# Kernel tuning notes

Hardware: AMD Instinct MI355X
Metric: run time of the kernel (lower is better)

The kernel has to match this reference:

```python
import jax, jax.numpy as jnp
import numpy as np

B, T, C, H = 4, 2048, 1024, 16
HD = C // H

def setup_inputs() -> dict:
    key = jax.random.key(0)
    ks = jax.random.split(key, 9)
    s = 1.0 / np.sqrt(C)
    return {
        'x':  jax.random.normal(ks[0], (B, T, C), jnp.float32),
        'Wq': jax.random.normal(ks[1], (C, C), jnp.float32) * s,
        'bq': jnp.zeros((C,), jnp.float32),
        'Wk': jax.random.normal(ks[2], (C, C), jnp.float32) * s,
        'bk': jnp.zeros((C,), jnp.float32),
        'Wv': jax.random.normal(ks[3], (C, C), jnp.float32) * s,
        'bv': jnp.zeros((C,), jnp.float32),
        'Wo': jax.random.normal(ks[4], (C, C), jnp.float32) * s,
        'bo': jnp.zeros((C,), jnp.float32),
    }

def reference(x, Wq, bq, Wk, bk, Wv, bv, Wo, bo):
    Bx, Tx, Cx = x.shape
    # projections (torch Linear: x @ W.T + b); split heads -> (B,H,T,HD)
    def heads(y):
        return y.reshape(Bx, Tx, H, HD).transpose(0, 2, 1, 3)
    q = heads(x @ Wq.T + bq)
    k = heads(x @ Wk.T + bk)
    v = heads(x @ Wv.T + bv)
    # NOTE: original scales by 1/sqrt(embedding_dim), not head_dim
    scale = 1.0 / jnp.sqrt(jnp.asarray(Cx, x.dtype))
    att = jnp.einsum('bhqd,bhkd->bhqk', q, k) * scale
    mask = jnp.tril(jnp.ones((Tx, Tx), dtype=bool))
    att = jnp.where(mask, att, jnp.asarray(-jnp.inf, att.dtype))
    att = jax.nn.softmax(att, axis=-1)
    y = jnp.einsum('bhqk,bhkd->bhqd', att, v)
    y = y.transpose(0, 2, 1, 3).reshape(Bx, Tx, Cx)
    return y @ Wo.T + bo
```

## Files before the change

### kernel.cpp

```cpp
#include <hip/hip_runtime.h>
#include <hip/hip_bf16.h>
#include <stdint.h>

#define NB 4
#define NT 2048
#define NC 1024
#define NH 16
#define NHD 64
#define NM (NB*NT)

typedef __attribute__((ext_vector_type(8))) __bf16 bf16x8;
typedef __attribute__((ext_vector_type(4))) float floatx4;
typedef __attribute__((ext_vector_type(8))) unsigned short ushortx8;

#define AS1(p) ((const __attribute__((address_space(1))) void*)(p))
#define AS3(p) ((__attribute__((address_space(3))) void*)(p))

__device__ __forceinline__ unsigned short f2bf(float f) {
    union { float f; unsigned int u; } v; v.f = f;
    unsigned int u = v.u;
    return (unsigned short)((u + 0x7FFFu + ((u >> 16) & 1u)) >> 16);
}
__device__ __forceinline__ unsigned int pk2(float lo, float hi) {
    union { float f; unsigned int u; } a, b; a.f = hi; b.f = lo;
    return __builtin_amdgcn_perm(a.u, b.u, 0x07060302u);
}


__global__ void cast_x_tiled(const float* __restrict__ in,
                             unsigned short* __restrict__ out, int ntiles) {
    const int wid  = (blockIdx.x * blockDim.x + threadIdx.x) >> 6;
    const int lane = threadIdx.x & 63;
    if (wid >= ntiles) return;
    const int R = wid >> 5, C = wid & 31;
    const float* src = in + ((size_t)(R*16 + (lane >> 2)))*1024 + C*32 + (lane & 3)*8;
    const floatx4 v0 = *(const floatx4*)src;
    const floatx4 v1 = *(const floatx4*)(src + 4);
    ushortx8 o;
    o[0] = f2bf(v0[0]); o[1] = f2bf(v0[1]); o[2] = f2bf(v0[2]); o[3] = f2bf(v0[3]);
    o[4] = f2bf(v1[0]); o[5] = f2bf(v1[1]); o[6] = f2bf(v1[2]); o[7] = f2bf(v1[3]);
    *(ushortx8*)&out[(size_t)wid*512 + (((lane & 3)*16 + (lane >> 2)))*8] = o;
}

__global__ void cast4_tiled(const float* __restrict__ w0, const float* __restrict__ w1,
                            const float* __restrict__ w2, const float* __restrict__ w3,
                            unsigned short* __restrict__ o0, unsigned short* __restrict__ o1,
                            unsigned short* __restrict__ o2, unsigned short* __restrict__ o3,
                            int ntiles) {
    const int wid  = (blockIdx.x * blockDim.x + threadIdx.x) >> 6;
    const int lane = threadIdx.x & 63;
    if (wid >= ntiles) return;
    const float* in; unsigned short* out;
    switch (blockIdx.y) {
        case 0: in = w0; out = o0; break;
        case 1: in = w1; out = o1; break;
        case 2: in = w2; out = o2; break;
        default: in = w3; out = o3; break;
    }
    const int R = wid >> 5, C = wid & 31;
    const float* src = in + ((size_t)(R*16 + (lane >> 2)))*1024 + C*32 + (lane & 3)*8;
    const floatx4 v0 = *(const floatx4*)src;
    const floatx4 v1 = *(const floatx4*)(src + 4);
    ushortx8 o;
    o[0] = f2bf(v0[0]); o[1] = f2bf(v0[1]); o[2] = f2bf(v0[2]); o[3] = f2bf(v0[3]);
    o[4] = f2bf(v1[0]); o[5] = f2bf(v1[1]); o[6] = f2bf(v1[2]); o[7] = f2bf(v1[3]);
    *(ushortx8*)&out[(size_t)wid*512 + (((lane & 3)*16 + (lane >> 2)))*8] = o;
}

#define TM 128
#define TN 128
#define BK 32

template<int MODE>
__device__ __forceinline__ void gemm_core(
    const unsigned short* __restrict__ A,
    const unsigned short* __restrict__ W,
    const float* __restrict__ bias,
    void* __restrict__ Out,
    unsigned short* As, unsigned short* Bs,
    int m_base, int n_base, float oscale)
{
    const int tid  = threadIdx.x;
    const int lane = tid & 63;
    const int wv   = tid >> 6;
    const int quad = lane >> 4;
    const int l16  = lane & 15;
    const int wm = (wv >> 1) * 64;
    const int wn = (wv & 1) * 64;

    floatx4 acc[4][4];
    #pragma unroll
    for (int i = 0; i < 4; ++i)
        #pragma unroll
        for (int j = 0; j < 4; ++j)
            acc[i][j] = (floatx4){0.f, 0.f, 0.f, 0.f};

    const int kTiles = NC / BK;
    const int kct = NC >> 5;

    const unsigned short* At = A + ((size_t)((m_base >> 4) + wv*2) * kct) * 512 + (size_t)lane*8;
    const unsigned short* Wt = W + ((size_t)((n_base >> 4) + wv*2) * kct) * 512 + (size_t)lane*8;
    const size_t rstride = (size_t)kct * 512;

    for (int kt = 0; kt < kTiles; ++kt) {
        __syncthreads();
        #pragma unroll
        for (int i = 0; i < 2; ++i) {
            __builtin_amdgcn_global_load_lds(
                AS1(At + (size_t)kt*512 + i*rstride),
                AS3(&As[(wv*2 + i)*512]), 16, 0, 0);
            __builtin_amdgcn_global_load_lds(
                AS1(Wt + (size_t)kt*512 + i*rstride),
                AS3(&Bs[(wv*2 + i)*512]), 16, 0, 0);
        }
        __syncthreads();

        bf16x8 af[4], bfr[4];
        #pragma unroll
        for (int mi = 0; mi < 4; ++mi)
            af[mi] = *(const bf16x8*)&As[((wv >> 1)*4 + mi)*512 + lane*8];
        #pragma unroll
        for (int ni = 0; ni < 4; ++ni)
            bfr[ni] = *(const bf16x8*)&Bs[((wv & 1)*4 + ni)*512 + lane*8];

        #pragma unroll
        for (int mi = 0; mi < 4; ++mi)
            #pragma unroll
            for (int ni = 0; ni < 4; ++ni) {
                if (MODE == 1)
                    acc[mi][ni] = __builtin_amdgcn_mfma_f32_16x16x32_bf16(
                        bfr[ni], af[mi], acc[mi][ni], 0, 0, 0);
                else
                    acc[mi][ni] = __builtin_amdgcn_mfma_f32_16x16x32_bf16(
                        af[mi], bfr[ni], acc[mi][ni], 0, 0, 0);
            }
    }

    #pragma unroll
    for (int mi = 0; mi < 4; ++mi) {
        #pragma unroll
        for (int ni = 0; ni < 4; ++ni) {
            if (MODE == 0) {
                const int col = n_base + wn + ni*16 + l16;
                const float bv = bias[col & 1023];
                #pragma unroll
                for (int r = 0; r < 4; ++r) {
                    const int row = m_base + wm + mi*16 + quad*4 + r;
                    ((float*)Out)[(size_t)row * NC + col] =
                        (acc[mi][ni][r] + bv) * oscale;
                }
            } else if (MODE == 1) {
                const int d0 = n_base + wn + ni*16 + quad*4;
                const int t  = m_base + wm + mi*16 + l16;
                const float4 b4 = *(const float4*)&bias[d0];
                const int bb = t >> 11, tt = t & (NT - 1);
                const int h  = (d0 >> 6) & (NH - 1), dd0 = d0 & 63;
                const int bh = bb * NH + h;
                const size_t idx0 =
                    ((size_t)((bh*128 + (tt >> 4))*2 + (dd0 >> 5)))*512
                    + (size_t)((((dd0 >> 3) & 3)*16 + (tt & 15))*8 + (dd0 & 7));
                ushort4 st;
                st.x = f2bf((acc[mi][ni][0] + b4.x) * oscale);
                st.y = f2bf((acc[mi][ni][1] + b4.y) * oscale);
                st.z = f2bf((acc[mi][ni][2] + b4.z) * oscale);
                st.w = f2bf((acc[mi][ni][3] + b4.w) * oscale);
                *(ushort4*)&((unsigned short*)Out)[idx0] = st;
            } else {
                const int col = n_base + wn + ni*16 + l16;
                const float bv = bias[col & 1023];
                const int row0 = m_base + wm + mi*16 + quad*4;
                const int bb = row0 >> 11, t0 = row0 & (NT - 1);
                const int h  = (col >> 6) & (NH - 1), hd = col & 63;
                const int bh = bb * NH + h;
                const int tk0 = t0 & 31;
                const int qv  = (tk0 >> 2) & 3;
                const int jv0 = (tk0 >> 4) << 2;
                const size_t idx0 =
                    ((size_t)((bh*64 + (t0 >> 5))*4 + (hd >> 4)))*512
                    + (size_t)((qv*16 + (hd & 15))*8 + jv0);
                ushort4 st;
                st.x = f2bf((acc[mi][ni][0] + bv) * oscale);
                st.y = f2bf((acc[mi][ni][1] + bv) * oscale);
                st.z = f2bf((acc[mi][ni][2] + bv) * oscale);
                st.w = f2bf((acc[mi][ni][3] + bv) * oscale);
                *(ushort4*)&((unsigned short*)Out)[idx0] = st;
            }
        }
    }
}

#define QSCALE (0.03125f * 1.44269504088896340736f)

__global__ __launch_bounds__(256) void gemm_qkv(
    const unsigned short* __restrict__ A,
    const unsigned short* __restrict__ Wq, const unsigned short* __restrict__ Wk,
    const unsigned short* __restrict__ Wv,
    const float* __restrict__ bq, const float* __restrict__ bk,
    const float* __restrict__ bv,
    unsigned short* __restrict__ Qo, unsigned short* __restrict__ Ko,
    unsigned short* __restrict__ Vo)
{
    __shared__ __align__(16) unsigned short As[TM*BK];
    __shared__ __align__(16) unsigned short Bs[TN*BK];
    const int wi = blockIdx.y >> 3;
    const int n_base = (blockIdx.y & 7) * TN;
    const int m_base = blockIdx.x * TM;
    if (wi == 0)
        gemm_core<1>(A, Wq, bq, Qo, As, Bs, m_base, n_base, QSCALE);
    else if (wi == 1)
        gemm_core<1>(A, Wk, bk, Ko, As, Bs, m_base, n_base, 1.0f);
    else
        gemm_core<2>(A, Wv, bv, Vo, As, Bs, m_base, n_base, 1.0f);
}

__global__ __launch_bounds__(256) void gemm_out(
    const unsigned short* __restrict__ A,
    const unsigned short* __restrict__ W,
    const float* __restrict__ bias,
    float* __restrict__ Out)
{
    __shared__ __align__(16) unsigned short As[TM*BK];
    __shared__ __align__(16) unsigned short Bs[TN*BK];
    gemm_core<0>(A, W, bias, Out, As, Bs, blockIdx.x * TM, blockIdx.y * TN, 1.0f);
}

__device__ __forceinline__ void attn_tile(
    const bf16x8 kf[4][2], const bf16x8 vf[4][2],
    const bf16x8 q[4], floatx4 o[2][4], float l[2],
    bool diag, int q0, int j0, int quad, int l16)
{
    #pragma unroll
    for (int sub = 0; sub < 2; ++sub) {
        const bf16x8 qx0 = q[sub*2];
        const bf16x8 qx1 = q[sub*2 + 1];

        floatx4 s[4];
        __builtin_amdgcn_s_setprio(1);
        #pragma unroll
        for (int ct = 0; ct < 4; ++ct) {
            s[ct] = (floatx4){0.f,0.f,0.f,0.f};
            s[ct] = __builtin_amdgcn_mfma_f32_16x16x32_bf16(kf[ct][0], qx0, s[ct], 0,0,0);
            s[ct] = __builtin_amdgcn_mfma_f32_16x16x32_bf16(kf[ct][1], qx1, s[ct], 0,0,0);
        }
        __builtin_amdgcn_s_setprio(0);

        float p[4][4];
        float lsum = 0.f;
        if (!diag) {
            #pragma unroll
            for (int ct = 0; ct < 4; ++ct)
                #pragma unroll
                for (int r = 0; r < 4; ++r) {
                    p[ct][r] = __builtin_amdgcn_exp2f(s[ct][r]);
                    lsum += p[ct][r];
                }
        } else {
            const int row = q0 + sub*16 + l16;
            #pragma unroll
            for (int ct = 0; ct < 4; ++ct)
                #pragma unroll
                for (int r = 0; r < 4; ++r) {
                    const int key = j0 + ct*16 + quad*4 + r;
                    p[ct][r] = (key <= row) ? __builtin_amdgcn_exp2f(s[ct][r]) : 0.f;
                    lsum += p[ct][r];
                }
        }
        l[sub] += lsum;

        union { bf16x8 v; unsigned int u[4]; } pf0, pf1;
        pf0.u[0] = pk2(p[0][0], p[0][1]); pf0.u[1] = pk2(p[0][2], p[0][3]);
        pf0.u[2] = pk2(p[1][0], p[1][1]); pf0.u[3] = pk2(p[1][2], p[1][3]);
        pf1.u[0] = pk2(p[2][0], p[2][1]); pf1.u[1] = pk2(p[2][2], p[2][3]);
        pf1.u[2] = pk2(p[3][0], p[3][1]); pf1.u[3] = pk2(p[3][2], p[3][3]);

        __builtin_amdgcn_s_setprio(1);
        #pragma unroll
        for (int nt = 0; nt < 4; ++nt) {
            o[sub][nt] = __builtin_amdgcn_mfma_f32_16x16x32_bf16(vf[nt][0], pf0.v, o[sub][nt], 0,0,0);
            o[sub][nt] = __builtin_amdgcn_mfma_f32_16x16x32_bf16(vf[nt][1], pf1.v, o[sub][nt], 0,0,0);
        }
        __builtin_amdgcn_s_setprio(0);
    }
}

__device__ __forceinline__ void attn_store(
    unsigned short* __restrict__ Y, const floatx4 o[2][4], const float l[2],
    int q0, int b, int h, int quad, int l16)
{
    float la = l[0], lb = l[1];
    la += __shfl_xor(la, 16); la += __shfl_xor(la, 32);
    lb += __shfl_xor(lb, 16); lb += __shfl_xor(lb, 32);
    const float ia = 1.0f / la, ib = 1.0f / lb;
    const size_t Rbase = (size_t)((b*NT + q0) >> 4);
    const int cg = (quad >> 1), co = (quad & 1)*4;
    #pragma unroll
    for (int nt = 0; nt < 4; ++nt) {
        const size_t base = ((Rbase*32 + h*2 + (nt >> 1))*512)
                          + (size_t)((((nt & 1)*2 + cg)*16 + l16)*8 + co);
        ushort4 wa, wb;
        wa.x = f2bf(o[0][nt][0]*ia); wa.y = f2bf(o[0][nt][1]*ia);
        wa.z = f2bf(o[0][nt][2]*ia); wa.w = f2bf(o[0][nt][3]*ia);
        wb.x = f2bf(o[1][nt][0]*ib); wb.y = f2bf(o[1][nt][1]*ib);
        wb.z = f2bf(o[1][nt][2]*ib); wb.w = f2bf(o[1][nt][3]*ib);
        *(ushort4*)&Y[base]         = wa;
        *(ushort4*)&Y[base + 16384] = wb;
    }
}

__device__ __forceinline__ void attn_pair(
    const unsigned short* __restrict__ Qf,
    const unsigned short* __restrict__ Kf,
    const unsigned short* __restrict__ Vf,
    unsigned short* __restrict__ Y,
    int bh, int stA, int stB, int lane)
{
    const int quad = lane >> 4, l16 = lane & 15;
    const int b = bh >> 4, h = bh & (NH - 1);
    const int q0A = stA * 32, q0B = stB * 32;
    const int FA = q0A >> 6, FB = q0B >> 6;

    const size_t qbA = ((size_t)(bh*128 + stA*2))*1024 + (size_t)lane*8;
    const size_t qbB = ((size_t)(bh*128 + stB*2))*1024 + (size_t)lane*8;
    bf16x8 qA[4], qB[4];
    qA[0] = *(const bf16x8*)&Qf[qbA];
    qA[1] = *(const bf16x8*)&Qf[qbA + 512];
    qA[2] = *(const bf16x8*)&Qf[qbA + 1024];
    qA[3] = *(const bf16x8*)&Qf[qbA + 1536];
    qB[0] = *(const bf16x8*)&Qf[qbB];
    qB[1] = *(const bf16x8*)&Qf[qbB + 512];
    qB[2] = *(const bf16x8*)&Qf[qbB + 1024];
    qB[3] = *(const bf16x8*)&Qf[qbB + 1536];

    const unsigned short* kp = Kf + (size_t)bh*131072 + (size_t)lane*8;
    const unsigned short* vp = Vf + (size_t)bh*131072 + (size_t)lane*8;

    floatx4 oA[2][4], oB[2][4];
    float lA[2] = {0.f, 0.f}, lB[2] = {0.f, 0.f};
    #pragma unroll
    for (int s2 = 0; s2 < 2; ++s2)
        #pragma unroll
        for (int nt = 0; nt < 4; ++nt) {
            oA[s2][nt] = (floatx4){0.f,0.f,0.f,0.f};
            oB[s2][nt] = (floatx4){0.f,0.f,0.f,0.f};
        }

    for (int f = 0; f <= FB; ++f) {
        const int j0 = f * 64;
        bf16x8 kf[4][2], vf[4][2];
        const unsigned short* kt = kp + (size_t)f * 4096;
        #pragma unroll
        for (int ct = 0; ct < 4; ++ct) {
            kf[ct][0] = *(const bf16x8*)&kt[ct*1024];
            kf[ct][1] = *(const bf16x8*)&kt[ct*1024 + 512];
        }
        const unsigned short* vt = vp + (size_t)f * 4096;
        #pragma unroll
        for (int nt = 0; nt < 4; ++nt) {
            vf[nt][0] = *(const bf16x8*)&vt[nt*512];
            vf[nt][1] = *(const bf16x8*)&vt[2048 + nt*512];
        }

        if (f <= FA)
            attn_tile(kf, vf, qA, oA, lA, f == FA, q0A, j0, quad, l16);
        attn_tile(kf, vf, qB, oB, lB, f == FB, q0B, j0, quad, l16);
    }

    attn_store(Y, oA, lA, q0A, b, h, quad, l16);
    attn_store(Y, oB, lB, q0B, b, h, quad, l16);
}

__global__ __launch_bounds__(256, 2) void flash_attn(
    const unsigned short* __restrict__ Qf,
    const unsigned short* __restrict__ Kf,
    const unsigned short* __restrict__ Vf,
    unsigned short* __restrict__ Y)
{
    const int tid  = threadIdx.x;
    const int wave = tid >> 6;
    const int lane = tid & 63;
    const int L  = blockIdx.x;
    const int bh = (L & 7) * 8 + ((L >> 3) & 7);
    const int x  = L >> 6;
    const int w  = x * 4 + wave;
    attn_pair(Qf, Kf, Vf, Y, bh, w, 63 - w, lane);
}

extern "C" void kernel_launch(void* const* d_in, const int* in_sizes, int n_in,
                              void* d_out, int out_size, void* d_ws, size_t ws_size,
                              hipStream_t stream) {
    const float* x  = (const float*)d_in[0];
    const float* Wq = (const float*)d_in[1];
    const float* bq = (const float*)d_in[2];
    const float* Wk = (const float*)d_in[3];
    const float* bk = (const float*)d_in[4];
    const float* Wv = (const float*)d_in[5];
    const float* bv = (const float*)d_in[6];
    const float* Wo = (const float*)d_in[7];
    const float* bo = (const float*)d_in[8];

    char* ws = (char*)d_ws;
    size_t off = 0;
    auto alloc = [&](size_t bytes) -> void* {
        void* p = ws + off;
        off += (bytes + 255) & ~(size_t)255;
        return p;
    };
    unsigned short* xb  = (unsigned short*)alloc((size_t)NM * NC * 2);
    unsigned short* Wqb = (unsigned short*)alloc((size_t)NC * NC * 2);
    unsigned short* Wkb = (unsigned short*)alloc((size_t)NC * NC * 2);
    unsigned short* Wvb = (unsigned short*)alloc((size_t)NC * NC * 2);
    unsigned short* Wob = (unsigned short*)alloc((size_t)NC * NC * 2);
    unsigned short* Qb  = (unsigned short*)alloc((size_t)NM * NC * 2);
    unsigned short* Kb  = (unsigned short*)alloc((size_t)NM * NC * 2);
    unsigned short* Vtb = (unsigned short*)alloc((size_t)NM * NC * 2);
    unsigned short* Yb  = (unsigned short*)alloc((size_t)NM * NC * 2);

    const int ntx = NM * NC / 512;
    const int ntw = NC * NC / 512;
    cast_x_tiled<<<(ntx*64 + 255)/256, 256, 0, stream>>>(x, xb, ntx);
    cast4_tiled<<<dim3((ntw*64 + 255)/256, 4), 256, 0, stream>>>(
        Wq, Wk, Wv, Wo, Wqb, Wkb, Wvb, Wob, ntw);

    gemm_qkv<<<dim3(NM / TM, 24), 256, 0, stream>>>(
        xb, Wqb, Wkb, Wvb, bq, bk, bv, Qb, Kb, Vtb);

    flash_attn<<<dim3(512), 256, 0, stream>>>(Qb, Kb, Vtb, Yb);

    gemm_out<<<dim3(NM / TM, NC / TN), 256, 0, stream>>>(Yb, Wob, bo, (float*)d_out);
}
```

Measured before the change: 233.9 us.

## Double-buffer GEMM LDS loads, skip masked attention subtiles, merge cast kernels

The GEMM core now double-buffers its LDS tiles. It issues the next k-tile's global-to-LDS loads before computing the current one and uses explicit vmcnt waits and barriers, so load latency overlaps with MFMA work. In flash attention, diagonal tiles whose query block sits in the lower half of a 64-key tile skip the upper 32 keys' QK and PV MFMAs and exps, since those keys are fully masked. The two fp32-to-bf16 cast kernels are merged into one launch. Double buffering doubles LDS use per GEMM block, which may reduce occupancy.

```diff
diff --git a/kernel.cpp b/kernel.cpp
--- a/kernel.cpp
+++ b/kernel.cpp
@@ -27,44 +27,35 @@
 }
 
 
-__global__ void cast_x_tiled(const float* __restrict__ in,
-                             unsigned short* __restrict__ out, int ntiles) {
+__global__ void cast_all(const float* __restrict__ x,
+                         const float* __restrict__ w0, const float* __restrict__ w1,
+                         const float* __restrict__ w2, const float* __restrict__ w3,
+                         unsigned short* __restrict__ xo,
+                         unsigned short* __restrict__ o0, unsigned short* __restrict__ o1,
+                         unsigned short* __restrict__ o2, unsigned short* __restrict__ o3)
+{
     const int wid  = (blockIdx.x * blockDim.x + threadIdx.x) >> 6;
     const int lane = threadIdx.x & 63;
-    if (wid >= ntiles) return;
-    const int R = wid >> 5, C = wid & 31;
+    const float* in; unsigned short* out; int tile;
+    if (wid < 16384) { in = x; out = xo; tile = wid; }
+    else {
+        const int t = wid - 16384;
+        tile = t & 2047;
+        switch (t >> 11) {
+            case 0: in = w0; out = o0; break;
+            case 1: in = w1; out = o1; break;
+            case 2: in = w2; out = o2; break;
+            default: in = w3; out = o3; break;
+        }
+    }
+    const int R = tile >> 5, C = tile & 31;
     const float* src = in + ((size_t)(R*16 + (lane >> 2)))*1024 + C*32 + (lane & 3)*8;
     const floatx4 v0 = *(const floatx4*)src;
     const floatx4 v1 = *(const floatx4*)(src + 4);
     ushortx8 o;
     o[0] = f2bf(v0[0]); o[1] = f2bf(v0[1]); o[2] = f2bf(v0[2]); o[3] = f2bf(v0[3]);
     o[4] = f2bf(v1[0]); o[5] = f2bf(v1[1]); o[6] = f2bf(v1[2]); o[7] = f2bf(v1[3]);
-    *(ushortx8*)&out[(size_t)wid*512 + (((lane & 3)*16 + (lane >> 2)))*8] = o;
-}
-
-__global__ void cast4_tiled(const float* __restrict__ w0, const float* __restrict__ w1,
-                            const float* __restrict__ w2, const float* __restrict__ w3,
-                            unsigned short* __restrict__ o0, unsigned short* __restrict__ o1,
-                            unsigned short* __restrict__ o2, unsigned short* __restrict__ o3,
-                            int ntiles) {
-    const int wid  = (blockIdx.x * blockDim.x + threadIdx.x) >> 6;
-    const int lane = threadIdx.x & 63;
-    if (wid >= ntiles) return;
-    const float* in; unsigned short* out;
-    switch (blockIdx.y) {
-        case 0: in = w0; out = o0; break;
-        case 1: in = w1; out = o1; break;
-        case 2: in = w2; out = o2; break;
-        default: in = w3; out = o3; break;
-    }
-    const int R = wid >> 5, C = wid & 31;
-    const float* src = in + ((size_t)(R*16 + (lane >> 2)))*1024 + C*32 + (lane & 3)*8;
-    const floatx4 v0 = *(const floatx4*)src;
-    const floatx4 v1 = *(const floatx4*)(src + 4);
-    ushortx8 o;
-    o[0] = f2bf(v0[0]); o[1] = f2bf(v0[1]); o[2] = f2bf(v0[2]); o[3] = f2bf(v0[3]);
-    o[4] = f2bf(v1[0]); o[5] = f2bf(v1[1]); o[6] = f2bf(v1[2]); o[7] = f2bf(v1[3]);
-    *(ushortx8*)&out[(size_t)wid*512 + (((lane & 3)*16 + (lane >> 2)))*8] = o;
+    *(ushortx8*)&out[(size_t)tile*512 + (((lane & 3)*16 + (lane >> 2)))*8] = o;
 }
 
 #define TM 128
@@ -95,33 +86,47 @@
         for (int j = 0; j < 4; ++j)
             acc[i][j] = (floatx4){0.f, 0.f, 0.f, 0.f};
 
-    const int kTiles = NC / BK;
     const int kct = NC >> 5;
 
     const unsigned short* At = A + ((size_t)((m_base >> 4) + wv*2) * kct) * 512 + (size_t)lane*8;
     const unsigned short* Wt = W + ((size_t)((n_base >> 4) + wv*2) * kct) * 512 + (size_t)lane*8;
     const size_t rstride = (size_t)kct * 512;
 
-    for (int kt = 0; kt < kTiles; ++kt) {
-        __syncthreads();
-        #pragma unroll
-        for (int i = 0; i < 2; ++i) {
-            __builtin_amdgcn_global_load_lds(
-                AS1(At + (size_t)kt*512 + i*rstride),
-                AS3(&As[(wv*2 + i)*512]), 16, 0, 0);
-            __builtin_amdgcn_global_load_lds(
-                AS1(Wt + (size_t)kt*512 + i*rstride),
-                AS3(&Bs[(wv*2 + i)*512]), 16, 0, 0);
-        }
-        __syncthreads();
+    #pragma unroll
+    for (int i = 0; i < 2; ++i) {
+        __builtin_amdgcn_global_load_lds(AS1(At + i*rstride),
+                                         AS3(&As[(wv*2 + i)*512]), 16, 0, 0);
+        __builtin_amdgcn_global_load_lds(AS1(Wt + i*rstride),
+                                         AS3(&Bs[(wv*2 + i)*512]), 16, 0, 0);
+    }
+
+    #pragma unroll 1
+    for (int kt = 0; kt < 32; ++kt) {
+        const int cur = (kt & 1) << 12;
+        const int nxt = 4096 - cur;
+        if (kt < 31) {
+            #pragma unroll
+            for (int i = 0; i < 2; ++i) {
+                __builtin_amdgcn_global_load_lds(
+                    AS1(At + (size_t)(kt+1)*512 + i*rstride),
+                    AS3(&As[nxt + (wv*2 + i)*512]), 16, 0, 0);
+                __builtin_amdgcn_global_load_lds(
+                    AS1(Wt + (size_t)(kt+1)*512 + i*rstride),
+                    AS3(&Bs[nxt + (wv*2 + i)*512]), 16, 0, 0);
+            }
+            asm volatile("s_waitcnt vmcnt(4)" ::: "memory");
+        } else {
+            asm volatile("s_waitcnt vmcnt(0)" ::: "memory");
+        }
+        __builtin_amdgcn_s_barrier();
 
         bf16x8 af[4], bfr[4];
         #pragma unroll
         for (int mi = 0; mi < 4; ++mi)
-            af[mi] = *(const bf16x8*)&As[((wv >> 1)*4 + mi)*512 + lane*8];
+            af[mi] = *(const bf16x8*)&As[cur + ((wv >> 1)*4 + mi)*512 + lane*8];
         #pragma unroll
         for (int ni = 0; ni < 4; ++ni)
-            bfr[ni] = *(const bf16x8*)&Bs[((wv & 1)*4 + ni)*512 + lane*8];
+            bfr[ni] = *(const bf16x8*)&Bs[cur + ((wv & 1)*4 + ni)*512 + lane*8];
 
         #pragma unroll
         for (int mi = 0; mi < 4; ++mi)
@@ -134,6 +139,7 @@
                     acc[mi][ni] = __builtin_amdgcn_mfma_f32_16x16x32_bf16(
                         af[mi], bfr[ni], acc[mi][ni], 0, 0, 0);
             }
+        __builtin_amdgcn_s_barrier();
     }
 
     #pragma unroll
@@ -200,8 +206,8 @@
     unsigned short* __restrict__ Qo, unsigned short* __restrict__ Ko,
     unsigned short* __restrict__ Vo)
 {
-    __shared__ __align__(16) unsigned short As[TM*BK];
-    __shared__ __align__(16) unsigned short Bs[TN*BK];
+    __shared__ __align__(16) unsigned short As[2*TM*BK];
+    __shared__ __align__(16) unsigned short Bs[2*TN*BK];
     const int wi = blockIdx.y >> 3;
     const int n_base = (blockIdx.y & 7) * TN;
     const int m_base = blockIdx.x * TM;
@@ -219,15 +225,15 @@
     const float* __restrict__ bias,
     float* __restrict__ Out)
 {
-    __shared__ __align__(16) unsigned short As[TM*BK];
-    __shared__ __align__(16) unsigned short Bs[TN*BK];
+    __shared__ __align__(16) unsigned short As[2*TM*BK];
+    __shared__ __align__(16) unsigned short Bs[2*TN*BK];
     gemm_core<0>(A, W, bias, Out, As, Bs, blockIdx.x * TM, blockIdx.y * TN, 1.0f);
 }
 
 __device__ __forceinline__ void attn_tile(
     const bf16x8 kf[4][2], const bf16x8 vf[4][2],
     const bf16x8 q[4], floatx4 o[2][4], float l[2],
-    bool diag, int q0, int j0, int quad, int l16)
+    bool diag, bool skiphi, int q0, int j0, int quad, int l16)
 {
     #pragma unroll
     for (int sub = 0; sub < 2; ++sub) {
@@ -237,27 +243,35 @@
         floatx4 s[4];
         __builtin_amdgcn_s_setprio(1);
         #pragma unroll
-        for (int ct = 0; ct < 4; ++ct) {
+        for (int ct = 0; ct < 2; ++ct) {
             s[ct] = (floatx4){0.f,0.f,0.f,0.f};
             s[ct] = __builtin_amdgcn_mfma_f32_16x16x32_bf16(kf[ct][0], qx0, s[ct], 0,0,0);
             s[ct] = __builtin_amdgcn_mfma_f32_16x16x32_bf16(kf[ct][1], qx1, s[ct], 0,0,0);
         }
+        if (!skiphi) {
+            #pragma unroll
+            for (int ct = 2; ct < 4; ++ct) {
+                s[ct] = (floatx4){0.f,0.f,0.f,0.f};
+                s[ct] = __builtin_amdgcn_mfma_f32_16x16x32_bf16(kf[ct][0], qx0, s[ct], 0,0,0);
+                s[ct] = __builtin_amdgcn_mfma_f32_16x16x32_bf16(kf[ct][1], qx1, s[ct], 0,0,0);
+            }
+        }
         __builtin_amdgcn_s_setprio(0);
 
         float p[4][4];
         float lsum = 0.f;
+        const int row = q0 + sub*16 + l16;
         if (!diag) {
             #pragma unroll
-            for (int ct = 0; ct < 4; ++ct)
+            for (int ct = 0; ct < 2; ++ct)
                 #pragma unroll
                 for (int r = 0; r < 4; ++r) {
                     p[ct][r] = __builtin_amdgcn_exp2f(s[ct][r]);
                     lsum += p[ct][r];
                 }
         } else {
-            const int row = q0 + sub*16 + l16;
-            #pragma unroll
-            for (int ct = 0; ct < 4; ++ct)
+            #pragma unroll
+            for (int ct = 0; ct < 2; ++ct)
                 #pragma unroll
                 for (int r = 0; r < 4; ++r) {
                     const int key = j0 + ct*16 + quad*4 + r;
@@ -265,21 +279,48 @@
                     lsum += p[ct][r];
                 }
         }
+        if (!skiphi) {
+            if (!diag) {
+                #pragma unroll
+                for (int ct = 2; ct < 4; ++ct)
+                    #pragma unroll
+                    for (int r = 0; r < 4; ++r) {
+                        p[ct][r] = __builtin_amdgcn_exp2f(s[ct][r]);
+                        lsum += p[ct][r];
+                    }
+            } else {
+                #pragma unroll
+                for (int ct = 2; ct < 4; ++ct)
+                    #pragma unroll
+                    for (int r = 0; r < 4; ++r) {
+                        const int key = j0 + ct*16 + quad*4 + r;
+                        p[ct][r] = (key <= row) ? __builtin_amdgcn_exp2f(s[ct][r]) : 0.f;
+                        lsum += p[ct][r];
+                    }
+            }
+        }
         l[sub] += lsum;
 
-        union { bf16x8 v; unsigned int u[4]; } pf0, pf1;
+        union { bf16x8 v; unsigned int u[4]; } pf0;
         pf0.u[0] = pk2(p[0][0], p[0][1]); pf0.u[1] = pk2(p[0][2], p[0][3]);
         pf0.u[2] = pk2(p[1][0], p[1][1]); pf0.u[3] = pk2(p[1][2], p[1][3]);
-        pf1.u[0] = pk2(p[2][0], p[2][1]); pf1.u[1] = pk2(p[2][2], p[2][3]);
-        pf1.u[2] = pk2(p[3][0], p[3][1]); pf1.u[3] = pk2(p[3][2], p[3][3]);
 
         __builtin_amdgcn_s_setprio(1);
         #pragma unroll
-        for (int nt = 0; nt < 4; ++nt) {
+        for (int nt = 0; nt < 4; ++nt)
             o[sub][nt] = __builtin_amdgcn_mfma_f32_16x16x32_bf16(vf[nt][0], pf0.v, o[sub][nt], 0,0,0);
-            o[sub][nt] = __builtin_amdgcn_mfma_f32_16x16x32_bf16(vf[nt][1], pf1.v, o[sub][nt], 0,0,0);
-        }
         __builtin_amdgcn_s_setprio(0);
+
+        if (!skiphi) {
+            union { bf16x8 v; unsigned int u[4]; } pf1;
+            pf1.u[0] = pk2(p[2][0], p[2][1]); pf1.u[1] = pk2(p[2][2], p[2][3]);
+            pf1.u[2] = pk2(p[3][0], p[3][1]); pf1.u[3] = pk2(p[3][2], p[3][3]);
+            __builtin_amdgcn_s_setprio(1);
+            #pragma unroll
+            for (int nt = 0; nt < 4; ++nt)
+                o[sub][nt] = __builtin_amdgcn_mfma_f32_16x16x32_bf16(vf[nt][1], pf1.v, o[sub][nt], 0,0,0);
+            __builtin_amdgcn_s_setprio(0);
+        }
     }
 }
 
@@ -318,6 +359,8 @@
     const int b = bh >> 4, h = bh & (NH - 1);
     const int q0A = stA * 32, q0B = stB * 32;
     const int FA = q0A >> 6, FB = q0B >> 6;
+    const bool skA = (q0A & 32) == 0;
+    const bool skB = (q0B & 32) == 0;
 
     const size_t qbA = ((size_t)(bh*128 + stA*2))*1024 + (size_t)lane*8;
     const size_t qbB = ((size_t)(bh*128 + stB*2))*1024 + (size_t)lane*8;
@@ -361,8 +404,10 @@
         }
 
         if (f <= FA)
-            attn_tile(kf, vf, qA, oA, lA, f == FA, q0A, j0, quad, l16);
-        attn_tile(kf, vf, qB, oB, lB, f == FB, q0B, j0, quad, l16);
+            attn_tile(kf, vf, qA, oA, lA, f == FA, (f == FA) && skA,
+                      q0A, j0, quad, l16);
+        attn_tile(kf, vf, qB, oB, lB, f == FB, (f == FB) && skB,
+                  q0B, j0, quad, l16);
     }
 
     attn_store(Y, oA, lA, q0A, b, h, quad, l16);
@@ -415,11 +460,8 @@
     unsigned short* Vtb = (unsigned short*)alloc((size_t)NM * NC * 2);
     unsigned short* Yb  = (unsigned short*)alloc((size_t)NM * NC * 2);
 
-    const int ntx = NM * NC / 512;
-    const int ntw = NC * NC / 512;
-    cast_x_tiled<<<(ntx*64 + 255)/256, 256, 0, stream>>>(x, xb, ntx);
-    cast4_tiled<<<dim3((ntw*64 + 255)/256, 4), 256, 0, stream>>>(
-        Wq, Wk, Wv, Wo, Wqb, Wkb, Wvb, Wob, ntw);
+    cast_all<<<(24576*64)/256, 256, 0, stream>>>(
+        x, Wq, Wk, Wv, Wo, xb, Wqb, Wkb, Wvb, Wob);
 
     gemm_qkv<<<dim3(NM / TM, 24), 256, 0, stream>>>(
         xb, Wqb, Wkb, Wvb, bq, bk, bv, Qb, Kb, Vtb);
```

New measurement: 233.8 us. No clear change (-0.1%).
